# Optimization experiments

Hardware: AMD Instinct MI355X
Metric: run time of the kernel (lower is better)

The kernel has to match this reference:

```python
import jax, jax.numpy as jnp
import numpy as np

LAMBDA_TEMP = 20.0
GAMMA = 20.0
MARGIN = 0.05
EPS = 1e-8

B, K, M, D = 128, 256, 8, 128


def _unit(x, axis=-1):
    return x / jnp.linalg.norm(x, axis=axis, keepdims=True)


def setup_inputs() -> dict:
    key = jax.random.key(0)
    k1, k2, k3 = jax.random.split(key, 3)
    v_proj = _unit(jax.random.normal(k1, (B, K, D), dtype=jnp.float32))
    prototypes = _unit(jax.random.normal(k2, (K, M, D), dtype=jnp.float32))
    concept_labels = jax.random.randint(k3, (B, K), 0, 2, dtype=jnp.int64)
    return {"v_proj": v_proj, "concept_labels": concept_labels, "prototypes": prototypes}


def reference(v_proj, concept_labels, prototypes):
    # all-pairs prototype similarities: query vector (b,k) vs prototypes of concept c
    # sims: (B, K, C, M)
    sims = jnp.einsum('bkd,cmd->bkcm', v_proj, prototypes)
    # Eq.6: soft assignment over the M prototypes of each concept
    q = jax.nn.softmax(GAMMA * sims, axis=-1)
    # Eq.7-8: weighted similarity sim_c(v)  -> (B, K, C)
    sim = jnp.sum(q * sims, axis=-1)
    # positive similarity: concept k queried against its own prototypes, plus margin
    sim_pos = jnp.einsum('bkk->bk', sim) + MARGIN  # (B, K)
    # Eq.9: -log( exp(lam*sim_pos) / (sum_c exp(lam*sim_c) + eps) )
    denom = jnp.sum(jnp.exp(LAMBDA_TEMP * sim), axis=-1) + EPS  # (B, K)
    loss_bk = jnp.log(denom) - LAMBDA_TEMP * sim_pos  # (B, K)
    mask = (concept_labels == 1).astype(loss_bk.dtype)
    num_pos = jnp.sum(mask)
    total = jnp.sum(loss_bk * mask)
    return jnp.where(num_pos > 0, total / num_pos, total)
```

## Files before the change

### kernel.cpp

```cpp
#include <hip/hip_runtime.h>

#define LT      20.0f
#define LN2     0.69314718055994531f
#define C2EXP   28.853900817779268f
#define CHUNKS  16
#define NBLK    1024

typedef _Float16 half8 __attribute__((ext_vector_type(8)));
typedef float    f32x4 __attribute__((ext_vector_type(4)));

#if __has_builtin(__builtin_amdgcn_exp2f)
#define EXP2F(x) __builtin_amdgcn_exp2f(x)
#else
#define EXP2F(x) __expf(0.69314718055994531f * (x))
#endif

__device__ __forceinline__ float swz16(float x) {
    return __int_as_float(__builtin_amdgcn_ds_swizzle(__float_as_int(x), 0x401F));
}

#define GLD16(gp, lp) __builtin_amdgcn_global_load_lds( \
    (const __attribute__((address_space(1))) void*)(gp), \
    (__attribute__((address_space(3))) void*)(lp), 16, 0, 0)

__global__ __launch_bounds__(256)
void mpcl_prep(const float* __restrict__ P, _Float16* __restrict__ Pw)
{
    int t    = blockIdx.x * 256 + threadIdx.x;
    int gcol = t >> 4;
    int dblk = t & 15;
    const float* src = P + ((size_t)gcol << 7) + dblk * 8;
    float4 a = *(const float4*)src;
    float4 b = *(const float4*)(src + 4);

    int ch   = gcol >> 7, col  = gcol & 127;
    int colq = col >> 5,  col5 = col & 31;
    int g = col5 >> 3, p = col5 & 7;
    int n = (g << 2) | (p & 3), h = p >> 2;
    int c = dblk >> 2, q = dblk & 3;
    int lane  = (q << 4) | n;
    int cfrag = (h << 2) | c;
    int slot  = ch * 2048 + colq * 512 + cfrag * 64 + lane;

    half8 hv;
    hv[0] = (_Float16)(C2EXP * a.x); hv[1] = (_Float16)(C2EXP * a.y);
    hv[2] = (_Float16)(C2EXP * a.z); hv[3] = (_Float16)(C2EXP * a.w);
    hv[4] = (_Float16)(C2EXP * b.x); hv[5] = (_Float16)(C2EXP * b.y);
    hv[6] = (_Float16)(C2EXP * b.z); hv[7] = (_Float16)(C2EXP * b.w);
    *(half8*)(Pw + (size_t)slot * 8) = hv;
}

__global__ __launch_bounds__(1024)
void mpcl_compact(const int* __restrict__ labels, int* __restrict__ ridx,
                  int* __restrict__ npos)
{
    __shared__ int wcnt[512];
    __shared__ int wsum[8];
    __shared__ int sbase[512];
    __shared__ int tot;
    const int tid = threadIdx.x, lane = tid & 63, w = tid >> 6;

    int lab[32];
#pragma unroll
    for (int i = 0; i < 32; ++i) lab[i] = labels[i * 1024 + tid];
#pragma unroll
    for (int i = 0; i < 32; ++i) {
        unsigned long long m = __ballot(lab[i] == 1);
        if (lane == 0) wcnt[i * 16 + w] = __popcll(m);
    }
    __syncthreads();

    int v = 0, orig = 0;
    if (tid < 512) { v = wcnt[tid]; orig = v; }
#pragma unroll
    for (int off = 1; off < 64; off <<= 1) {
        int t = __shfl_up(v, off);
        if (lane >= off) v += t;
    }
    if (lane == 63 && w < 8) wsum[w] = v;
    __syncthreads();
    if (tid == 0) {
        int acc = 0;
#pragma unroll
        for (int i = 0; i < 8; ++i) { int t = wsum[i]; wsum[i] = acc; acc += t; }
        tot = acc; npos[0] = acc;
    }
    __syncthreads();
    if (tid < 512) sbase[tid] = v - orig + wsum[w];
    __syncthreads();

#pragma unroll
    for (int i = 0; i < 32; ++i) {
        unsigned long long m = __ballot(lab[i] == 1);
        int pos = sbase[i * 16 + w] + __popcll(m & ((1ull << lane) - 1));
        if (lab[i] == 1) ridx[pos] = i * 1024 + tid;
    }
    for (int j = tot + tid; j < 32768; j += 1024) ridx[j] = 0;
}

__global__ __attribute__((amdgpu_flat_work_group_size(512, 512),
                          amdgpu_waves_per_eu(4, 4)))
void mpcl_main(const float* __restrict__ V,
               const _Float16* __restrict__ Pw,
               const int* __restrict__ ridx,
               const int* __restrict__ npos,
               float* __restrict__ part)
{
    __shared__ __align__(16) _Float16 Pst[2][2048 * 8];
    __shared__ float sh_denom[32];
    __shared__ float sh_simpos[32];

    const int np = *npos;
    const int rowbase = blockIdx.x * 32;
    if (rowbase >= np) return;

    const int tid  = threadIdx.x;
    const int lane = tid & 63;
    const int w    = tid >> 6;
    const int colq = w & 3;
    const int rg   = w >> 2;
    const int n    = lane & 15;
    const int q    = lane >> 4;

    if (tid < 32) { sh_denom[tid] = 0.0f; sh_simpos[tid] = 0.0f; }

    const _Float16* gbase = Pw + (size_t)(w * 256 + lane) * 8;

#define STAGE(CH, B) do {                                       \
    const _Float16* g_ = gbase + (size_t)(CH) * 16384;          \
    _Float16* l_ = &Pst[B][(w * 256) * 8];                      \
    GLD16(g_,        l_);                                       \
    GLD16(g_ +  512, l_ +  512);                                \
    GLD16(g_ + 1024, l_ + 1024);                                \
    GLD16(g_ + 1536, l_ + 1536);                                \
} while (0)

    const int myrow = ridx[rowbase + rg * 16 + n];
    half8 vh[4];
    {
        const float* vr = V + ((size_t)myrow << 7) + q * 8;
#pragma unroll
        for (int c = 0; c < 4; ++c) {
            float4 x0 = *(const float4*)(vr + c * 32);
            float4 x1 = *(const float4*)(vr + c * 32 + 4);
            vh[c][0] = (_Float16)x0.x; vh[c][1] = (_Float16)x0.y;
            vh[c][2] = (_Float16)x0.z; vh[c][3] = (_Float16)x0.w;
            vh[c][4] = (_Float16)x1.x; vh[c][5] = (_Float16)x1.y;
            vh[c][6] = (_Float16)x1.z; vh[c][7] = (_Float16)x1.w;
        }
    }
    __syncthreads();

    STAGE(0, 0);
    STAGE(1, 1);

    const int rowk = myrow & 255;
    const int aoff = (colq * 512 + lane) * 8;

    float dn = 0.f;
    int cA = colq * 4 + q;

#pragma unroll 1
    for (int ch = 0; ch < CHUNKS; ++ch) {
        if (ch < CHUNKS - 1) asm volatile("s_waitcnt vmcnt(4)" ::: "memory");
        else                 asm volatile("s_waitcnt vmcnt(0)" ::: "memory");
        __builtin_amdgcn_s_barrier();

        const _Float16* base = &Pst[ch & 1][0];

        f32x4 acc1 = {0.f, 0.f, 0.f, 0.f};
        f32x4 acc2 = {0.f, 0.f, 0.f, 0.f};
#pragma unroll
        for (int c = 0; c < 4; ++c) {
            half8 a1 = *(const half8*)&base[aoff + c * 512];
            half8 a2 = *(const half8*)&base[aoff + c * 512 + 2048];
            acc1 = __builtin_amdgcn_mfma_f32_16x16x32_f16(a1, vh[c], acc1, 0, 0, 0);
            acc2 = __builtin_amdgcn_mfma_f32_16x16x32_f16(a2, vh[c], acc2, 0, 0, 0);
        }

        asm volatile("s_waitcnt lgkmcnt(0)" ::: "memory");
        __builtin_amdgcn_s_barrier();
        if (ch + 2 < CHUNKS) STAGE(ch + 2, ch & 1);

        {
            float x0 = acc1[0], x1 = acc1[1], x2 = acc1[2], x3 = acc1[3];
            float x4 = acc2[0], x5 = acc2[1], x6 = acc2[2], x7 = acc2[3];
            float e0 = EXP2F(x0), e1 = EXP2F(x1), e2 = EXP2F(x2), e3 = EXP2F(x3);
            float e4 = EXP2F(x4), e5 = EXP2F(x5), e6 = EXP2F(x6), e7 = EXP2F(x7);
            float es = ((e0 + e1) + (e2 + e3)) + ((e4 + e5) + (e6 + e7));
            float ss = fmaf(e0, x0, fmaf(e1, x1, fmaf(e2, x2, e3 * x3)))
                     + fmaf(e4, x4, fmaf(e5, x5, fmaf(e6, x6, e7 * x7)));
            float simY = __fdividef(ss, es);
            dn += EXP2F(simY);
            if (cA == rowk)
                sh_simpos[rg * 16 + n] = simY;
        }
        cA += 16;
    }

    {
        float t = dn;
        t += swz16(t);
        t += __shfl_xor(t, 32);
        if (lane < 16)
            atomicAdd(&sh_denom[rg * 16 + n], t);
    }
    __syncthreads();

    if (w == 0) {
        float s = 0.f, cc = 0.f;
        if (lane < 32 && rowbase + lane < np) {
            s  = logf(sh_denom[lane] + 1e-8f) - LN2 * sh_simpos[lane] - 1.0f;
            cc = 1.0f;
        }
#pragma unroll
        for (int off = 32; off >= 1; off >>= 1) {
            s  += __shfl_down(s, off);
            cc += __shfl_down(cc, off);
        }
        if (lane == 0) {
            part[2 * blockIdx.x]     = s;
            part[2 * blockIdx.x + 1] = cc;
        }
    }
}

__global__ __launch_bounds__(512)
void mpcl_finish(const float* __restrict__ part, const int* __restrict__ npos,
                 float* __restrict__ out)
{
    __shared__ float sh[16];
    const int tid  = threadIdx.x;
    const int lane = tid & 63;
    const int w    = tid >> 6;
    const int nact = (*npos + 31) >> 5;

    float s = 0.f, cc = 0.f;
    for (int i = tid; i < nact; i += 512) {
        s  += part[2 * i];
        cc += part[2 * i + 1];
    }
#pragma unroll
    for (int off = 32; off >= 1; off >>= 1) {
        s  += __shfl_down(s, off);
        cc += __shfl_down(cc, off);
    }
    if (lane == 0) { sh[w] = s; sh[8 + w] = cc; }
    __syncthreads();
    if (tid == 0) {
        float ts = 0.f, tc = 0.f;
#pragma unroll
        for (int i = 0; i < 8; ++i) { ts += sh[i]; tc += sh[8 + i]; }
        out[0] = (tc > 0.0f) ? (ts / tc) : ts;
    }
}

extern "C" void kernel_launch(void* const* d_in, const int* in_sizes, int n_in,
                              void* d_out, int out_size, void* d_ws, size_t ws_size,
                              hipStream_t stream)
{
    const float* V      = (const float*)d_in[0];
    const int*   labels = (const int*)d_in[1];
    const float* P      = (const float*)d_in[2];
    float* out = (float*)d_out;

    int*      npos = (int*)d_ws;
    float*    part = (float*)((char*)d_ws + 256);
    int*      ridx = (int*)((char*)d_ws + 16384);
    _Float16* Pw   = (_Float16*)((char*)d_ws + 262144);

    mpcl_prep<<<128, 256, 0, stream>>>(P, Pw);
    mpcl_compact<<<1, 1024, 0, stream>>>(labels, ridx, npos);
    mpcl_main<<<NBLK, 512, 0, stream>>>(V, Pw, ridx, npos, part);
    mpcl_finish<<<1, 512, 0, stream>>>(part, npos, out);
}
```

Baseline: 93.68 us.

## Split concept range across block pairs and process 64 rows per block

Each block now handles 64 query rows, two 16-row fragments per wave-group, so every staged prototype tile feeds twice as many MFMAs. The 256 concepts are split in half between paired blocks, which keeps the block count and parallelism unchanged while halving the chunk loop per block. Per-row partial denominators and the positive similarity go to a workspace array, and the finish kernel combines the halves and applies the log per row. This costs more registers, a larger workspace, and a finish kernel that has to walk every positive row.

Result: slower. 99.15 us (+5.8%).

```diff
diff --git a/kernel.cpp b/kernel.cpp
--- a/kernel.cpp
+++ b/kernel.cpp
@@ -3,7 +3,7 @@
 #define LT      20.0f
 #define LN2     0.69314718055994531f
 #define C2EXP   28.853900817779268f
-#define CHUNKS  16
+#define CHUNKS_H 8
 #define NBLK    1024
 
 typedef _Float16 half8 __attribute__((ext_vector_type(8)));
@@ -104,14 +104,15 @@
                const _Float16* __restrict__ Pw,
                const int* __restrict__ ridx,
                const int* __restrict__ npos,
-               float* __restrict__ part)
+               float* __restrict__ dnw)
 {
     __shared__ __align__(16) _Float16 Pst[2][2048 * 8];
-    __shared__ float sh_denom[32];
-    __shared__ float sh_simpos[32];
+    __shared__ float sh_denom[64];
+    __shared__ float sh_simpos[64];
 
     const int np = *npos;
-    const int rowbase = blockIdx.x * 32;
+    const int h  = blockIdx.x & 1;
+    const int rowbase = (blockIdx.x >> 1) * 64;
     if (rowbase >= np) return;
 
     const int tid  = threadIdx.x;
@@ -122,9 +123,10 @@
     const int n    = lane & 15;
     const int q    = lane >> 4;
 
-    if (tid < 32) { sh_denom[tid] = 0.0f; sh_simpos[tid] = 0.0f; }
-
-    const _Float16* gbase = Pw + (size_t)(w * 256 + lane) * 8;
+    if (tid < 64) { sh_denom[tid] = 0.0f; sh_simpos[tid] = 0.0f; }
+
+    const _Float16* gbase = Pw + (size_t)h * (CHUNKS_H * 16384)
+                               + (size_t)(w * 256 + lane) * 8;
 
 #define STAGE(CH, B) do {                                       \
     const _Float16* g_ = gbase + (size_t)(CH) * 16384;          \
@@ -135,18 +137,21 @@
     GLD16(g_ + 1536, l_ + 1536);                                \
 } while (0)
 
-    const int myrow = ridx[rowbase + rg * 16 + n];
-    half8 vh[4];
-    {
-        const float* vr = V + ((size_t)myrow << 7) + q * 8;
+    int myrow[2];
+    half8 vh[2][4];
+#pragma unroll
+    for (int rf = 0; rf < 2; ++rf) {
+        int pos = rowbase + rg * 32 + rf * 16 + n;
+        myrow[rf] = ridx[pos < np ? pos : np - 1];
+        const float* vr = V + ((size_t)myrow[rf] << 7) + q * 8;
 #pragma unroll
         for (int c = 0; c < 4; ++c) {
             float4 x0 = *(const float4*)(vr + c * 32);
             float4 x1 = *(const float4*)(vr + c * 32 + 4);
-            vh[c][0] = (_Float16)x0.x; vh[c][1] = (_Float16)x0.y;
-            vh[c][2] = (_Float16)x0.z; vh[c][3] = (_Float16)x0.w;
-            vh[c][4] = (_Float16)x1.x; vh[c][5] = (_Float16)x1.y;
-            vh[c][6] = (_Float16)x1.z; vh[c][7] = (_Float16)x1.w;
+            vh[rf][c][0] = (_Float16)x0.x; vh[rf][c][1] = (_Float16)x0.y;
+            vh[rf][c][2] = (_Float16)x0.z; vh[rf][c][3] = (_Float16)x0.w;
+            vh[rf][c][4] = (_Float16)x1.x; vh[rf][c][5] = (_Float16)x1.y;
+            vh[rf][c][6] = (_Float16)x1.z; vh[rf][c][7] = (_Float16)x1.w;
         }
     }
     __syncthreads();
@@ -154,104 +159,97 @@
     STAGE(0, 0);
     STAGE(1, 1);
 
-    const int rowk = myrow & 255;
-    const int aoff = (colq * 512 + lane) * 8;
-
-    float dn = 0.f;
-    int cA = colq * 4 + q;
+    const int rowk0 = myrow[0] & 255;
+    const int rowk1 = myrow[1] & 255;
+    const int aoff  = (colq * 512 + lane) * 8;
+
+    float dn0 = 0.f, dn1 = 0.f;
+    int cA = h * 128 + colq * 4 + q;
 
 #pragma unroll 1
-    for (int ch = 0; ch < CHUNKS; ++ch) {
-        if (ch < CHUNKS - 1) asm volatile("s_waitcnt vmcnt(4)" ::: "memory");
-        else                 asm volatile("s_waitcnt vmcnt(0)" ::: "memory");
+    for (int ch = 0; ch < CHUNKS_H; ++ch) {
+        if (ch < CHUNKS_H - 1) asm volatile("s_waitcnt vmcnt(4)" ::: "memory");
+        else                   asm volatile("s_waitcnt vmcnt(0)" ::: "memory");
         __builtin_amdgcn_s_barrier();
 
         const _Float16* base = &Pst[ch & 1][0];
 
-        f32x4 acc1 = {0.f, 0.f, 0.f, 0.f};
-        f32x4 acc2 = {0.f, 0.f, 0.f, 0.f};
+        f32x4 acc1[2] = {{0.f,0.f,0.f,0.f},{0.f,0.f,0.f,0.f}};
+        f32x4 acc2[2] = {{0.f,0.f,0.f,0.f},{0.f,0.f,0.f,0.f}};
 #pragma unroll
         for (int c = 0; c < 4; ++c) {
             half8 a1 = *(const half8*)&base[aoff + c * 512];
             half8 a2 = *(const half8*)&base[aoff + c * 512 + 2048];
-            acc1 = __builtin_amdgcn_mfma_f32_16x16x32_f16(a1, vh[c], acc1, 0, 0, 0);
-            acc2 = __builtin_amdgcn_mfma_f32_16x16x32_f16(a2, vh[c], acc2, 0, 0, 0);
+            acc1[0] = __builtin_amdgcn_mfma_f32_16x16x32_f16(a1, vh[0][c], acc1[0], 0, 0, 0);
+            acc1[1] = __builtin_amdgcn_mfma_f32_16x16x32_f16(a1, vh[1][c], acc1[1], 0, 0, 0);
+            acc2[0] = __builtin_amdgcn_mfma_f32_16x16x32_f16(a2, vh[0][c], acc2[0], 0, 0, 0);
+            acc2[1] = __builtin_amdgcn_mfma_f32_16x16x32_f16(a2, vh[1][c], acc2[1], 0, 0, 0);
         }
 
         asm volatile("s_waitcnt lgkmcnt(0)" ::: "memory");
         __builtin_amdgcn_s_barrier();
-        if (ch + 2 < CHUNKS) STAGE(ch + 2, ch & 1);
-
-        {
-            float x0 = acc1[0], x1 = acc1[1], x2 = acc1[2], x3 = acc1[3];
-            float x4 = acc2[0], x5 = acc2[1], x6 = acc2[2], x7 = acc2[3];
+        if (ch + 2 < CHUNKS_H) STAGE(ch + 2, ch & 1);
+
+#pragma unroll
+        for (int rf = 0; rf < 2; ++rf) {
+            float x0 = acc1[rf][0], x1 = acc1[rf][1], x2 = acc1[rf][2], x3 = acc1[rf][3];
+            float x4 = acc2[rf][0], x5 = acc2[rf][1], x6 = acc2[rf][2], x7 = acc2[rf][3];
             float e0 = EXP2F(x0), e1 = EXP2F(x1), e2 = EXP2F(x2), e3 = EXP2F(x3);
             float e4 = EXP2F(x4), e5 = EXP2F(x5), e6 = EXP2F(x6), e7 = EXP2F(x7);
             float es = ((e0 + e1) + (e2 + e3)) + ((e4 + e5) + (e6 + e7));
             float ss = fmaf(e0, x0, fmaf(e1, x1, fmaf(e2, x2, e3 * x3)))
                      + fmaf(e4, x4, fmaf(e5, x5, fmaf(e6, x6, e7 * x7)));
             float simY = __fdividef(ss, es);
-            dn += EXP2F(simY);
-            if (cA == rowk)
-                sh_simpos[rg * 16 + n] = simY;
+            if (rf) dn1 += EXP2F(simY); else dn0 += EXP2F(simY);
+            if (cA == (rf ? rowk1 : rowk0))
+                sh_simpos[rg * 32 + rf * 16 + n] = simY;
         }
         cA += 16;
     }
 
-    {
-        float t = dn;
+#pragma unroll
+    for (int rf = 0; rf < 2; ++rf) {
+        float t = rf ? dn1 : dn0;
         t += swz16(t);
         t += __shfl_xor(t, 32);
         if (lane < 16)
-            atomicAdd(&sh_denom[rg * 16 + n], t);
+            atomicAdd(&sh_denom[rg * 32 + rf * 16 + n], t);
     }
     __syncthreads();
 
     if (w == 0) {
-        float s = 0.f, cc = 0.f;
-        if (lane < 32 && rowbase + lane < np) {
-            s  = logf(sh_denom[lane] + 1e-8f) - LN2 * sh_simpos[lane] - 1.0f;
-            cc = 1.0f;
-        }
-#pragma unroll
-        for (int off = 32; off >= 1; off >>= 1) {
-            s  += __shfl_down(s, off);
-            cc += __shfl_down(cc, off);
-        }
-        if (lane == 0) {
-            part[2 * blockIdx.x]     = s;
-            part[2 * blockIdx.x + 1] = cc;
-        }
-    }
-}
-
-__global__ __launch_bounds__(512)
-void mpcl_finish(const float* __restrict__ part, const int* __restrict__ npos,
+        int pos = rowbase + lane;
+        int mr  = ridx[pos < np ? pos : np - 1];
+        dnw[h * 32768 + pos] = sh_denom[lane];
+        if (((mr & 255) >> 7) == h)
+            dnw[65536 + pos] = sh_simpos[lane];
+    }
+}
+
+__global__ __launch_bounds__(1024)
+void mpcl_finish(const float* __restrict__ dnw, const int* __restrict__ npos,
                  float* __restrict__ out)
 {
     __shared__ float sh[16];
     const int tid  = threadIdx.x;
     const int lane = tid & 63;
     const int w    = tid >> 6;
-    const int nact = (*npos + 31) >> 5;
-
-    float s = 0.f, cc = 0.f;
-    for (int i = tid; i < nact; i += 512) {
-        s  += part[2 * i];
-        cc += part[2 * i + 1];
-    }
-#pragma unroll
-    for (int off = 32; off >= 1; off >>= 1) {
-        s  += __shfl_down(s, off);
-        cc += __shfl_down(cc, off);
-    }
-    if (lane == 0) { sh[w] = s; sh[8 + w] = cc; }
+    const int np   = *npos;
+
+    float s = 0.f;
+    for (int i = tid; i < np; i += 1024) {
+        float dn = dnw[i] + dnw[32768 + i];
+        s += logf(dn + 1e-8f) - LN2 * dnw[65536 + i] - 1.0f;
+    }
+#pragma unroll
+    for (int off = 32; off >= 1; off >>= 1) s += __shfl_down(s, off);
+    if (lane == 0) sh[w] = s;
     __syncthreads();
     if (tid == 0) {
-        float ts = 0.f, tc = 0.f;
-#pragma unroll
-        for (int i = 0; i < 8; ++i) { ts += sh[i]; tc += sh[8 + i]; }
-        out[0] = (tc > 0.0f) ? (ts / tc) : ts;
+        float ts = 0.f;
+#pragma unroll
+        for (int i = 0; i < 16; ++i) ts += sh[i];
+        out[0] = (np > 0) ? (ts / (float)np) : 0.0f;
     }
 }
 
@@ -265,12 +263,12 @@
     float* out = (float*)d_out;
 
     int*      npos = (int*)d_ws;
-    float*    part = (float*)((char*)d_ws + 256);
-    int*      ridx = (int*)((char*)d_ws + 16384);
-    _Float16* Pw   = (_Float16*)((char*)d_ws + 262144);
+    float*    dnw  = (float*)((char*)d_ws + 4096);
+    int*      ridx = (int*)((char*)d_ws + 397312);
+    _Float16* Pw   = (_Float16*)((char*)d_ws + 528384);
 
     mpcl_prep<<<128, 256, 0, stream>>>(P, Pw);
     mpcl_compact<<<1, 1024, 0, stream>>>(labels, ridx, npos);
-    mpcl_main<<<NBLK, 512, 0, stream>>>(V, Pw, ridx, npos, part);
-    mpcl_finish<<<1, 512, 0, stream>>>(part, npos, out);
-}
+    mpcl_main<<<NBLK, 512, 0, stream>>>(V, Pw, ridx, npos, dnw);
+    mpcl_finish<<<1, 1024, 0, stream>>>(dnw, npos, out);
+}
```

## Switch to 32x32x16 MFMA with per-wave private LDS tiles and merge prep kernels

Applied to the files above, without the earlier changes.

The main kernel moves from 16x16x32 MFMAs on 512-thread blocks to 32x32x16 MFMAs on 256-thread blocks. Each wave now stages and consumes its own slice of the prototype chunk, which removes both block-wide barriers from the chunk loop. The prototype repacking is rewritten to match the new fragment layout, and the prep and compaction kernels are fused into one 33-block launch to save a kernel launch. In exchange, each wave issues twice as many async loads and holds more vector registers for V and the two 16-wide accumulators, which could reduce occupancy.

Measured after the change: 93.97 us. About the same (+0.3%).

```diff
diff --git a/kernel.cpp b/kernel.cpp
--- a/kernel.cpp
+++ b/kernel.cpp
@@ -6,8 +6,8 @@
 #define CHUNKS  16
 #define NBLK    1024
 
-typedef _Float16 half8 __attribute__((ext_vector_type(8)));
-typedef float    f32x4 __attribute__((ext_vector_type(4)));
+typedef _Float16 half8  __attribute__((ext_vector_type(8)));
+typedef float    f32x16 __attribute__((ext_vector_type(16)));
 
 #if __has_builtin(__builtin_amdgcn_exp2f)
 #define EXP2F(x) __builtin_amdgcn_exp2f(x)
@@ -15,90 +15,86 @@
 #define EXP2F(x) __expf(0.69314718055994531f * (x))
 #endif
 
-__device__ __forceinline__ float swz16(float x) {
-    return __int_as_float(__builtin_amdgcn_ds_swizzle(__float_as_int(x), 0x401F));
-}
-
 #define GLD16(gp, lp) __builtin_amdgcn_global_load_lds( \
     (const __attribute__((address_space(1))) void*)(gp), \
     (__attribute__((address_space(3))) void*)(lp), 16, 0, 0)
 
-__global__ __launch_bounds__(256)
-void mpcl_prep(const float* __restrict__ P, _Float16* __restrict__ Pw)
-{
-    int t    = blockIdx.x * 256 + threadIdx.x;
-    int gcol = t >> 4;
-    int dblk = t & 15;
-    const float* src = P + ((size_t)gcol << 7) + dblk * 8;
-    float4 a = *(const float4*)src;
-    float4 b = *(const float4*)(src + 4);
-
-    int ch   = gcol >> 7, col  = gcol & 127;
-    int colq = col >> 5,  col5 = col & 31;
-    int g = col5 >> 3, p = col5 & 7;
-    int n = (g << 2) | (p & 3), h = p >> 2;
-    int c = dblk >> 2, q = dblk & 3;
-    int lane  = (q << 4) | n;
-    int cfrag = (h << 2) | c;
-    int slot  = ch * 2048 + colq * 512 + cfrag * 64 + lane;
-
-    half8 hv;
-    hv[0] = (_Float16)(C2EXP * a.x); hv[1] = (_Float16)(C2EXP * a.y);
-    hv[2] = (_Float16)(C2EXP * a.z); hv[3] = (_Float16)(C2EXP * a.w);
-    hv[4] = (_Float16)(C2EXP * b.x); hv[5] = (_Float16)(C2EXP * b.y);
-    hv[6] = (_Float16)(C2EXP * b.z); hv[7] = (_Float16)(C2EXP * b.w);
-    *(half8*)(Pw + (size_t)slot * 8) = hv;
-}
 
 __global__ __launch_bounds__(1024)
-void mpcl_compact(const int* __restrict__ labels, int* __restrict__ ridx,
-                  int* __restrict__ npos)
+void mpcl_prep_compact(const float* __restrict__ P,
+                       const int*   __restrict__ labels,
+                       _Float16* __restrict__ Pw,
+                       int* __restrict__ ridx, int* __restrict__ npos)
 {
     __shared__ int wcnt[512];
     __shared__ int wsum[8];
     __shared__ int sbase[512];
     __shared__ int tot;
-    const int tid = threadIdx.x, lane = tid & 63, w = tid >> 6;
-
-    int lab[32];
-#pragma unroll
-    for (int i = 0; i < 32; ++i) lab[i] = labels[i * 1024 + tid];
-#pragma unroll
-    for (int i = 0; i < 32; ++i) {
-        unsigned long long m = __ballot(lab[i] == 1);
-        if (lane == 0) wcnt[i * 16 + w] = __popcll(m);
-    }
-    __syncthreads();
-
-    int v = 0, orig = 0;
-    if (tid < 512) { v = wcnt[tid]; orig = v; }
-#pragma unroll
-    for (int off = 1; off < 64; off <<= 1) {
-        int t = __shfl_up(v, off);
-        if (lane >= off) v += t;
-    }
-    if (lane == 63 && w < 8) wsum[w] = v;
-    __syncthreads();
-    if (tid == 0) {
-        int acc = 0;
-#pragma unroll
-        for (int i = 0; i < 8; ++i) { int t = wsum[i]; wsum[i] = acc; acc += t; }
-        tot = acc; npos[0] = acc;
-    }
-    __syncthreads();
-    if (tid < 512) sbase[tid] = v - orig + wsum[w];
-    __syncthreads();
-
-#pragma unroll
-    for (int i = 0; i < 32; ++i) {
-        unsigned long long m = __ballot(lab[i] == 1);
-        int pos = sbase[i * 16 + w] + __popcll(m & ((1ull << lane) - 1));
-        if (lab[i] == 1) ridx[pos] = i * 1024 + tid;
-    }
-    for (int j = tot + tid; j < 32768; j += 1024) ridx[j] = 0;
-}
-
-__global__ __attribute__((amdgpu_flat_work_group_size(512, 512),
+
+    if (blockIdx.x < 32) {
+        int t    = blockIdx.x * 1024 + threadIdx.x;
+        int gcol = t >> 4;
+        int dblk = t & 15;
+        const float* src = P + ((size_t)gcol << 7) + dblk * 8;
+        float4 x0 = *(const float4*)src;
+        float4 x1 = *(const float4*)(src + 4);
+
+        int ch = gcol >> 7, col = gcol & 127;
+        int g  = col >> 5,  col5 = col & 31;
+        int cl = col5 >> 3, p = col5 & 7;
+        int a  = (p & 3) | ((cl & 1) << 2) | ((cl >> 1) << 3) | ((p >> 2) << 4);
+        int hi = dblk & 1, s = dblk >> 1;
+        int l  = (hi << 5) | a;
+        int slot = ch * 2048 + (g * 8 + s) * 64 + l;
+
+        half8 hv;
+        hv[0] = (_Float16)(C2EXP * x0.x); hv[1] = (_Float16)(C2EXP * x0.y);
+        hv[2] = (_Float16)(C2EXP * x0.z); hv[3] = (_Float16)(C2EXP * x0.w);
+        hv[4] = (_Float16)(C2EXP * x1.x); hv[5] = (_Float16)(C2EXP * x1.y);
+        hv[6] = (_Float16)(C2EXP * x1.z); hv[7] = (_Float16)(C2EXP * x1.w);
+        *(half8*)(Pw + (size_t)slot * 8) = hv;
+    } else {
+        const int tid = threadIdx.x, lane = tid & 63, w = tid >> 6;
+        int lab[32];
+#pragma unroll
+        for (int i = 0; i < 32; ++i) lab[i] = labels[i * 1024 + tid];
+#pragma unroll
+        for (int i = 0; i < 32; ++i) {
+            unsigned long long m = __ballot(lab[i] == 1);
+            if (lane == 0) wcnt[i * 16 + w] = __popcll(m);
+        }
+        __syncthreads();
+
+        int v = 0, orig = 0;
+        if (tid < 512) { v = wcnt[tid]; orig = v; }
+#pragma unroll
+        for (int off = 1; off < 64; off <<= 1) {
+            int t2 = __shfl_up(v, off);
+            if (lane >= off) v += t2;
+        }
+        if (lane == 63 && w < 8) wsum[w] = v;
+        __syncthreads();
+        if (tid == 0) {
+            int acc = 0;
+#pragma unroll
+            for (int i = 0; i < 8; ++i) { int t2 = wsum[i]; wsum[i] = acc; acc += t2; }
+            tot = acc; npos[0] = acc;
+        }
+        __syncthreads();
+        if (tid < 512) sbase[tid] = v - orig + wsum[w];
+        __syncthreads();
+
+#pragma unroll
+        for (int i = 0; i < 32; ++i) {
+            unsigned long long m = __ballot(lab[i] == 1);
+            int pos = sbase[i * 16 + w] + __popcll(m & ((1ull << lane) - 1));
+            if (lab[i] == 1) ridx[pos] = i * 1024 + tid;
+        }
+        for (int j = tot + tid; j < 32768; j += 1024) ridx[j] = 0;
+    }
+}
+
+__global__ __attribute__((amdgpu_flat_work_group_size(256, 256),
                           amdgpu_waves_per_eu(4, 4)))
 void mpcl_main(const float* __restrict__ V,
                const _Float16* __restrict__ Pw,
@@ -106,7 +102,7 @@
                const int* __restrict__ npos,
                float* __restrict__ part)
 {
-    __shared__ __align__(16) _Float16 Pst[2][2048 * 8];
+    __shared__ __align__(16) _Float16 Pst[2][16384];
     __shared__ float sh_denom[32];
     __shared__ float sh_simpos[32];
 
@@ -114,103 +110,107 @@
     const int rowbase = blockIdx.x * 32;
     if (rowbase >= np) return;
 
-    const int tid  = threadIdx.x;
-    const int lane = tid & 63;
-    const int w    = tid >> 6;
-    const int colq = w & 3;
-    const int rg   = w >> 2;
-    const int n    = lane & 15;
-    const int q    = lane >> 4;
-
-    if (tid < 32) { sh_denom[tid] = 0.0f; sh_simpos[tid] = 0.0f; }
-
-    const _Float16* gbase = Pw + (size_t)(w * 256 + lane) * 8;
+    const int tid = threadIdx.x;
+    const int l   = tid & 63;
+    const int w   = tid >> 6;
+    const int a   = l & 31;
+    const int hi  = l >> 5;
+
+    if (tid < 32) sh_denom[tid] = 0.0f;
+
+    const int pos   = rowbase + a;
+    const int myrow = ridx[pos < np ? pos : np - 1];
+    const int rowk  = myrow & 255;
+
+    half8 vh[8];
+    {
+        const float* vr = V + ((size_t)myrow << 7) + hi * 8;
+#pragma unroll
+        for (int s = 0; s < 8; ++s) {
+            float4 x0 = *(const float4*)(vr + s * 16);
+            float4 x1 = *(const float4*)(vr + s * 16 + 4);
+            vh[s][0] = (_Float16)x0.x; vh[s][1] = (_Float16)x0.y;
+            vh[s][2] = (_Float16)x0.z; vh[s][3] = (_Float16)x0.w;
+            vh[s][4] = (_Float16)x1.x; vh[s][5] = (_Float16)x1.y;
+            vh[s][6] = (_Float16)x1.z; vh[s][7] = (_Float16)x1.w;
+        }
+    }
+    __syncthreads();
+
+    const _Float16* gbase = Pw + (size_t)(w * 512 + l) * 8;
 
 #define STAGE(CH, B) do {                                       \
     const _Float16* g_ = gbase + (size_t)(CH) * 16384;          \
-    _Float16* l_ = &Pst[B][(w * 256) * 8];                      \
-    GLD16(g_,        l_);                                       \
-    GLD16(g_ +  512, l_ +  512);                                \
-    GLD16(g_ + 1024, l_ + 1024);                                \
-    GLD16(g_ + 1536, l_ + 1536);                                \
+    _Float16* l_ = &Pst[B][w * 4096];                           \
+    GLD16(g_,        l_);        GLD16(g_ +  512, l_ +  512);   \
+    GLD16(g_ + 1024, l_ + 1024); GLD16(g_ + 1536, l_ + 1536);   \
+    GLD16(g_ + 2048, l_ + 2048); GLD16(g_ + 2560, l_ + 2560);   \
+    GLD16(g_ + 3072, l_ + 3072); GLD16(g_ + 3584, l_ + 3584);   \
 } while (0)
-
-    const int myrow = ridx[rowbase + rg * 16 + n];
-    half8 vh[4];
-    {
-        const float* vr = V + ((size_t)myrow << 7) + q * 8;
-#pragma unroll
-        for (int c = 0; c < 4; ++c) {
-            float4 x0 = *(const float4*)(vr + c * 32);
-            float4 x1 = *(const float4*)(vr + c * 32 + 4);
-            vh[c][0] = (_Float16)x0.x; vh[c][1] = (_Float16)x0.y;
-            vh[c][2] = (_Float16)x0.z; vh[c][3] = (_Float16)x0.w;
-            vh[c][4] = (_Float16)x1.x; vh[c][5] = (_Float16)x1.y;
-            vh[c][6] = (_Float16)x1.z; vh[c][7] = (_Float16)x1.w;
-        }
-    }
-    __syncthreads();
 
     STAGE(0, 0);
     STAGE(1, 1);
 
-    const int rowk = myrow & 255;
-    const int aoff = (colq * 512 + lane) * 8;
-
     float dn = 0.f;
-    int cA = colq * 4 + q;
+
+#define SOFT8(y0,y1,y2,y3,y4,y5,y6,y7, CONCEPT) do {                        \
+    float e0=EXP2F(y0), e1=EXP2F(y1), e2=EXP2F(y2), e3=EXP2F(y3);           \
+    float e4=EXP2F(y4), e5=EXP2F(y5), e6=EXP2F(y6), e7=EXP2F(y7);           \
+    float es = ((e0+e1)+(e2+e3)) + ((e4+e5)+(e6+e7));                       \
+    float ss = fmaf(e0,y0, fmaf(e1,y1, fmaf(e2,y2, e3*y3)))                 \
+             + fmaf(e4,y4, fmaf(e5,y5, fmaf(e6,y6, e7*y7)));                \
+    float simY = __fdividef(ss, es);                   \
+    dn += EXP2F(simY);                                                      \
+    if ((CONCEPT) == rowk) sh_simpos[a] = simY; \
+} while (0)
 
 #pragma unroll 1
     for (int ch = 0; ch < CHUNKS; ++ch) {
-        if (ch < CHUNKS - 1) asm volatile("s_waitcnt vmcnt(4)" ::: "memory");
+        if (ch < CHUNKS - 1) asm volatile("s_waitcnt vmcnt(8)" ::: "memory");
         else                 asm volatile("s_waitcnt vmcnt(0)" ::: "memory");
-        __builtin_amdgcn_s_barrier();
-
-        const _Float16* base = &Pst[ch & 1][0];
-
-        f32x4 acc1 = {0.f, 0.f, 0.f, 0.f};
-        f32x4 acc2 = {0.f, 0.f, 0.f, 0.f};
-#pragma unroll
-        for (int c = 0; c < 4; ++c) {
-            half8 a1 = *(const half8*)&base[aoff + c * 512];
-            half8 a2 = *(const half8*)&base[aoff + c * 512 + 2048];
-            acc1 = __builtin_amdgcn_mfma_f32_16x16x32_f16(a1, vh[c], acc1, 0, 0, 0);
-            acc2 = __builtin_amdgcn_mfma_f32_16x16x32_f16(a2, vh[c], acc2, 0, 0, 0);
-        }
-
+
+        const _Float16* bs = &Pst[ch & 1][w * 4096];
+        f32x16 acA = {0.f,0.f,0.f,0.f,0.f,0.f,0.f,0.f,0.f,0.f,0.f,0.f,0.f,0.f,0.f,0.f};
+        f32x16 acB = {0.f,0.f,0.f,0.f,0.f,0.f,0.f,0.f,0.f,0.f,0.f,0.f,0.f,0.f,0.f,0.f};
+        {
+            half8 p0 = *(const half8*)&bs[l * 8];
+            half8 p4 = *(const half8*)&bs[l * 8 + 4 * 512];
+            acA = __builtin_amdgcn_mfma_f32_32x32x16_f16(p0, vh[0], acA, 0, 0, 0);
+            acB = __builtin_amdgcn_mfma_f32_32x32x16_f16(p4, vh[4], acB, 0, 0, 0);
+            half8 p1 = *(const half8*)&bs[l * 8 + 1 * 512];
+            half8 p5 = *(const half8*)&bs[l * 8 + 5 * 512];
+            acA = __builtin_amdgcn_mfma_f32_32x32x16_f16(p1, vh[1], acA, 0, 0, 0);
+            acB = __builtin_amdgcn_mfma_f32_32x32x16_f16(p5, vh[5], acB, 0, 0, 0);
+            half8 p2 = *(const half8*)&bs[l * 8 + 2 * 512];
+            half8 p6 = *(const half8*)&bs[l * 8 + 6 * 512];
+            acA = __builtin_amdgcn_mfma_f32_32x32x16_f16(p2, vh[2], acA, 0, 0, 0);
+            acB = __builtin_amdgcn_mfma_f32_32x32x16_f16(p6, vh[6], acB, 0, 0, 0);
+            half8 p3 = *(const half8*)&bs[l * 8 + 3 * 512];
+            half8 p7 = *(const half8*)&bs[l * 8 + 7 * 512];
+            acA = __builtin_amdgcn_mfma_f32_32x32x16_f16(p3, vh[3], acA, 0, 0, 0);
+            acB = __builtin_amdgcn_mfma_f32_32x32x16_f16(p7, vh[7], acB, 0, 0, 0);
+        }
         asm volatile("s_waitcnt lgkmcnt(0)" ::: "memory");
-        __builtin_amdgcn_s_barrier();
         if (ch + 2 < CHUNKS) STAGE(ch + 2, ch & 1);
 
-        {
-            float x0 = acc1[0], x1 = acc1[1], x2 = acc1[2], x3 = acc1[3];
-            float x4 = acc2[0], x5 = acc2[1], x6 = acc2[2], x7 = acc2[3];
-            float e0 = EXP2F(x0), e1 = EXP2F(x1), e2 = EXP2F(x2), e3 = EXP2F(x3);
-            float e4 = EXP2F(x4), e5 = EXP2F(x5), e6 = EXP2F(x6), e7 = EXP2F(x7);
-            float es = ((e0 + e1) + (e2 + e3)) + ((e4 + e5) + (e6 + e7));
-            float ss = fmaf(e0, x0, fmaf(e1, x1, fmaf(e2, x2, e3 * x3)))
-                     + fmaf(e4, x4, fmaf(e5, x5, fmaf(e6, x6, e7 * x7)));
-            float simY = __fdividef(ss, es);
-            dn += EXP2F(simY);
-            if (cA == rowk)
-                sh_simpos[rg * 16 + n] = simY;
-        }
-        cA += 16;
+        f32x16 acc = acA + acB;
+        const int cb = (ch << 4) + (w << 2) + hi;
+        SOFT8(acc[0], acc[1], acc[2],  acc[3],  acc[8],  acc[9],  acc[10], acc[11], cb);
+        SOFT8(acc[4], acc[5], acc[6],  acc[7],  acc[12], acc[13], acc[14], acc[15], cb + 2);
     }
 
     {
         float t = dn;
-        t += swz16(t);
         t += __shfl_xor(t, 32);
-        if (lane < 16)
-            atomicAdd(&sh_denom[rg * 16 + n], t);
+        if (hi == 0)
+            atomicAdd(&sh_denom[a], t);
     }
     __syncthreads();
 
     if (w == 0) {
         float s = 0.f, cc = 0.f;
-        if (lane < 32 && rowbase + lane < np) {
-            s  = logf(sh_denom[lane] + 1e-8f) - LN2 * sh_simpos[lane] - 1.0f;
+        if (l < 32 && rowbase + l < np) {
+            s  = logf(sh_denom[l] + 1e-8f) - LN2 * sh_simpos[l] - 1.0f;
             cc = 1.0f;
         }
 #pragma unroll
@@ -218,7 +218,7 @@
             s  += __shfl_down(s, off);
             cc += __shfl_down(cc, off);
         }
-        if (lane == 0) {
+        if (l == 0) {
             part[2 * blockIdx.x]     = s;
             part[2 * blockIdx.x + 1] = cc;
         }
@@ -267,10 +267,9 @@
     int*      npos = (int*)d_ws;
     float*    part = (float*)((char*)d_ws + 256);
     int*      ridx = (int*)((char*)d_ws + 16384);
-    _Float16* Pw   = (_Float16*)((char*)d_ws + 262144);
-
-    mpcl_prep<<<128, 256, 0, stream>>>(P, Pw);
-    mpcl_compact<<<1, 1024, 0, stream>>>(labels, ridx, npos);
-    mpcl_main<<<NBLK, 512, 0, stream>>>(V, Pw, ridx, npos, part);
+    _Float16* Pw   = (_Float16*)((char*)d_ws + 147456);
+
+    mpcl_prep_compact<<<33, 1024, 0, stream>>>(P, labels, Pw, ridx, npos);
+    mpcl_main<<<NBLK, 256, 0, stream>>>(V, Pw, ridx, npos, part);
     mpcl_finish<<<1, 512, 0, stream>>>(part, npos, out);
 }
```
